# Kernel tuning notes

Hardware: AMD Instinct MI355X
Metric: run time of the kernel (lower is better)

## Reference

```python
import jax, jax.numpy as jnp
import numpy as np

TOP_K = 3


def setup_inputs() -> dict:
    key = jax.random.key(0)
    k1, k2, k3 = jax.random.split(key, 3)
    N, M, D = 100000, 6890, 128
    source_feats = jax.random.normal(k1, (N, D), dtype=jnp.float32)
    target_feats = jax.random.normal(k2, (M, D), dtype=jnp.float32)
    target_points = jax.random.normal(k3, (M, 3), dtype=jnp.float32)
    return {
        "source_feats": source_feats,
        "target_feats": target_feats,
        "target_points": target_points,
    }


def reference(source_feats, target_feats, target_points):
    # Pairwise squared distances via matmul + squared norms: [N, M]
    dp = jnp.matmul(source_feats, target_feats.T)
    source_sq = jnp.sum(source_feats * source_feats, axis=-1, keepdims=True)  # [N,1]
    target_sq = jnp.sum(target_feats * target_feats, axis=-1)                 # [M]
    dists = source_sq - 2.0 * dp + target_sq[None, :]
    # top-3 nearest neighbors (topk of negated distances, like torch.topk(-dists))
    scores, indices = jax.lax.top_k(-dists, TOP_K)      # [N,3], [N,3]
    weights = jax.nn.softmax(scores, axis=-1)           # [N,3]
    selected = target_points[indices]                   # [N,3,3] gather
    predicted_points = jnp.sum(selected * weights[..., None], axis=-2)  # [N,3]
    return predicted_points
```

## Files before the change

### kernel.cpp

```cpp
#include <hip/hip_runtime.h>
#include <math.h>

#define D 128
#define CT 2
#define SRCS_PER_WAVE (CT * 16)
#define WAVES 4
#define BIAS 16.0f
#define REFK 10
#define TILEB 8192
#define BUFB  8448

typedef __attribute__((ext_vector_type(8))) short short8;
typedef __attribute__((ext_vector_type(4))) float f32x4;

static __device__ __forceinline__ unsigned short f2bf(float x) {
    unsigned u = __float_as_uint(x);
    unsigned r = u + 0x7FFFu + ((u >> 16) & 1u);
    return (unsigned short)(r >> 16);
}

static __device__ __forceinline__ unsigned med3u(unsigned a, unsigned b, unsigned c) {
    unsigned d;
    asm("v_med3_u32 %0, %1, %2, %3" : "=v"(d) : "v"(a), "v"(b), "v"(c));
    return d;
}

static __device__ __forceinline__ void ins5(unsigned st[5], unsigned k) {
    st[4] = med3u(st[4], st[3], k);
    st[3] = med3u(st[3], st[2], k);
    st[2] = med3u(st[2], st[1], k);
    st[1] = med3u(st[1], st[0], k);
    st[0] = st[0] < k ? st[0] : k;
}

static __device__ __forceinline__ void ins10(unsigned st[REFK], unsigned k) {
    #pragma unroll
    for (int s = REFK - 1; s >= 1; --s) st[s] = med3u(st[s], st[s - 1], k);
    st[0] = st[0] < k ? st[0] : k;
}

static __device__ __forceinline__ void gload_lds16(const void* g, void* l) {
    __builtin_amdgcn_global_load_lds(
        (const __attribute__((address_space(1))) unsigned*)g,
        (__attribute__((address_space(3))) unsigned*)l, 16, 0, 0);
}
static __device__ __forceinline__ void gload_lds4(const void* g, void* l) {
    __builtin_amdgcn_global_load_lds(
        (const __attribute__((address_space(1))) unsigned*)g,
        (__attribute__((address_space(3))) unsigned*)l, 4, 0, 0);
}

__global__ void prep_kernel(const float* __restrict__ tgt, unsigned short* __restrict__ tbf,
                            float* __restrict__ tsqb, float* __restrict__ tsqe,
                            int M, int Mpad) {
    int row  = blockIdx.x;
    int lane = threadIdx.x;
    if (row >= Mpad) return;
    float2 v = make_float2(0.f, 0.f);
    if (row < M) v = *(const float2*)(tgt + (size_t)row * D + lane * 2);
    unsigned pack = (unsigned)f2bf(-2.f * v.x) | ((unsigned)f2bf(-2.f * v.y) << 16);
    size_t byte = (size_t)row * 256 + (size_t)(((lane >> 2) ^ (row & 15)) * 16 + (lane & 3) * 4);
    *(unsigned*)((char*)tbf + byte) = pack;
    float ss = v.x * v.x + v.y * v.y;
    #pragma unroll
    for (int off = 1; off < 64; off <<= 1) ss += __shfl_xor(ss, off);
    if (lane == 0) {
        tsqe[row] = ss;
        tsqb[row] = (row < M) ? (ss + BIAS) : __builtin_inff();
    }
}

__global__ __launch_bounds__(256, 4)
void knn_scan(const float* __restrict__ src, const unsigned short* __restrict__ tbf,
              const float* __restrict__ tsqb, unsigned* __restrict__ keys,
              int N, int M, int h0, int msteps) {
    const int tid  = (int)threadIdx.x;
    const int wid  = tid >> 6;
    const int lane = tid & 63;
    const int c16  = lane & 15;
    const int g    = lane >> 4;
    const int half = blockIdx.y;
    const int colbase = blockIdx.x * (WAVES * SRCS_PER_WAVE) + wid * SRCS_PER_WAVE;

    __shared__ __align__(16) char smem[3 * BUFB];

    short8 bfrag[CT][4];
    #pragma unroll
    for (int ct = 0; ct < CT; ++ct) {
        int srow = colbase + ct * 16 + c16;
        if (srow >= N) srow = N - 1;
        const float* sp = src + (size_t)srow * D + g * 8;
        #pragma unroll
        for (int kk = 0; kk < 4; ++kk) {
            float4 v0 = *(const float4*)(sp + kk * 32);
            float4 v1 = *(const float4*)(sp + kk * 32 + 4);
            short8 b;
            b[0] = (short)f2bf(v0.x); b[1] = (short)f2bf(v0.y);
            b[2] = (short)f2bf(v0.z); b[3] = (short)f2bf(v0.w);
            b[4] = (short)f2bf(v1.x); b[5] = (short)f2bf(v1.y);
            b[6] = (short)f2bf(v1.z); b[7] = (short)f2bf(v1.w);
            bfrag[ct][kk] = b;
        }
    }

    unsigned st[CT][5];
    #pragma unroll
    for (int ct = 0; ct < CT; ++ct)
        #pragma unroll
        for (int s = 0; s < 5; ++s) st[ct][s] = 0xFFFFFFFFu;

    int oe[4];
    #pragma unroll
    for (int kk = 0; kk < 4; ++kk) oe[kk] = c16 * 16 + ((g + 4 * kk) ^ c16);

    const int t0 = half ? h0 : 0;
    const int tc = half ? (msteps - h0) : h0;
    const int tlast = t0 + tc - 1;

    #define STAGE(tile, b)                                                          \
        do {                                                                        \
            const char* gb_ = (const char*)tbf + (size_t)(tile) * TILEB;            \
            char* lb_ = smem + (size_t)(b) * BUFB;                                  \
            gload_lds16(gb_ + wid * 2048 + lane * 16, lb_ + wid * 2048);            \
            gload_lds16(gb_ + wid * 2048 + 1024 + lane * 16, lb_ + wid * 2048 + 1024);\
            gload_lds4((const char*)tsqb + (size_t)(tile) * 128 + lane * 4,         \
                       lb_ + TILEB);                                                \
        } while (0)

    #define COMPUTE(b)                                                              \
        do {                                                                        \
            const short8* A_ = (const short8*)(smem + (size_t)(b) * BUFB);          \
            const float*  Q_ = (const float*)(smem + (size_t)(b) * BUFB + TILEB);   \
            _Pragma("unroll")                                                       \
            for (int sub_ = 0; sub_ < 2; ++sub_) {                                  \
                short8 a_[4];                                                       \
                _Pragma("unroll")                                                   \
                for (int kk = 0; kk < 4; ++kk) a_[kk] = A_[sub_ * 256 + oe[kk]];    \
                float4 q_ = *(const float4*)(Q_ + sub_ * 16 + g * 4);               \
                _Pragma("unroll")                                                   \
                for (int ct = 0; ct < CT; ++ct) {                                   \
                    f32x4 acc = { q_.x, q_.y, q_.z, q_.w };                         \
                    _Pragma("unroll")                                               \
                    for (int kk = 0; kk < 4; ++kk)                                  \
                        acc = __builtin_amdgcn_mfma_f32_16x16x32_bf16(              \
                                  a_[kk], bfrag[ct][kk], acc, 0, 0, 0);             \
                    _Pragma("unroll")                                               \
                    for (int e = 0; e < 4; ++e) {                                   \
                        unsigned key = (__float_as_uint(acc[e]) & 0xFFFFE000u)      \
                                       | (jb + (unsigned)e);                        \
                        ins5(st[ct], key);                                          \
                    }                                                               \
                }                                                                   \
                jb += 16;                                                           \
            }                                                                       \
        } while (0)

    unsigned jb = (unsigned)(t0 * 32 + g * 4);

    STAGE(t0, 0);
    STAGE(t0 + 1, 1);
    asm volatile("s_waitcnt vmcnt(3)\n\ts_barrier" ::: "memory");

    for (int i = 0; i < tc; i += 3) {
        int t_ = t0 + i;
        int s2 = t_ + 2 < tlast ? t_ + 2 : tlast;
        int s3 = t_ + 3 < tlast ? t_ + 3 : tlast;
        int s4 = t_ + 4 < tlast ? t_ + 4 : tlast;
        STAGE(s2, 2);
        COMPUTE(0);
        asm volatile("s_waitcnt vmcnt(3)\n\ts_barrier" ::: "memory");
        STAGE(s3, 0);
        COMPUTE(1);
        asm volatile("s_waitcnt vmcnt(3)\n\ts_barrier" ::: "memory");
        STAGE(s4, 1);
        COMPUTE(2);
        asm volatile("s_waitcnt vmcnt(3)\n\ts_barrier" ::: "memory");
    }
    asm volatile("s_waitcnt vmcnt(0)" ::: "memory");
    #undef STAGE
    #undef COMPUTE

    #pragma unroll
    for (int ct = 0; ct < CT; ++ct) {
        int srow = colbase + ct * 16 + c16;
        if (srow < N) {
            #pragma unroll
            for (int s = 0; s < 5; ++s)
                keys[(size_t)srow * 40 + half * 20 + g * 5 + s] = st[ct][s];
        }
    }
}

__global__ __launch_bounds__(256, 4)
void knn_merge(const float* __restrict__ src, const float* __restrict__ tgt,
               const float* __restrict__ tsqe, const unsigned* __restrict__ keys,
               const float* __restrict__ tpts, float* __restrict__ out,
               int N, int M) {
    int i = blockIdx.x * 256 + (int)threadIdx.x;
    if (i >= N) return;

    unsigned best[REFK];
    #pragma unroll
    for (int s = 0; s < REFK; ++s) best[s] = 0xFFFFFFFFu;

    const uint4* kp = (const uint4*)(keys + (size_t)i * 40);
    #pragma unroll
    for (int q = 0; q < 10; ++q) {
        uint4 kv = kp[q];
        ins10(best, kv.x); ins10(best, kv.y); ins10(best, kv.z); ins10(best, kv.w);
    }

    int js[REFK]; float dt[REFK];
    #pragma unroll
    for (int s = 0; s < REFK; ++s) {
        int j = (int)(best[s] & 0x1FFFu);
        js[s] = (j < M) ? j : (M - 1);
        dt[s] = 0.f;
    }

    const float4* sp = (const float4*)(src + (size_t)i * D);
    for (int kc = 0; kc < D / 4; ++kc) {
        float4 sv = sp[kc];
        #pragma unroll
        for (int s = 0; s < REFK; ++s) {
            float4 tv = *(const float4*)(tgt + (size_t)js[s] * D + kc * 4);
            dt[s] = fmaf(sv.x, tv.x, fmaf(sv.y, tv.y, fmaf(sv.z, tv.z, fmaf(sv.w, tv.w, dt[s]))));
        }
    }

    float d0 = __builtin_inff(), d1 = d0, d2 = d0;
    int i0 = 0, i1 = 0, i2 = 0;
    #pragma unroll
    for (int s = 0; s < REFK; ++s) {
        float dd = fmaf(-2.f, dt[s], tsqe[js[s]]);
        int jj = js[s];
        if (dd < d2) {
            if (dd < d1) {
                d2 = d1; i2 = i1;
                if (dd < d0) { d1 = d0; i1 = i0; d0 = dd; i0 = jj; }
                else         { d1 = dd; i1 = jj; }
            } else { d2 = dd; i2 = jj; }
        }
    }

    float e1 = __expf(d0 - d1);
    float e2 = __expf(d0 - d2);
    float inv = 1.f / (1.f + e1 + e2);
    float w0 = inv, w1 = e1 * inv, w2 = e2 * inv;
    const float* p0 = tpts + 3 * (size_t)i0;
    const float* p1 = tpts + 3 * (size_t)i1;
    const float* p2 = tpts + 3 * (size_t)i2;
    out[3 * (size_t)i + 0] = w0 * p0[0] + w1 * p1[0] + w2 * p2[0];
    out[3 * (size_t)i + 1] = w0 * p0[1] + w1 * p1[1] + w2 * p2[1];
    out[3 * (size_t)i + 2] = w0 * p0[2] + w1 * p1[2] + w2 * p2[2];
}

extern "C" void kernel_launch(void* const* d_in, const int* in_sizes, int n_in,
                              void* d_out, int out_size, void* d_ws, size_t ws_size,
                              hipStream_t stream) {
    const float* src  = (const float*)d_in[0];
    const float* tgt  = (const float*)d_in[1];
    const float* tpts = (const float*)d_in[2];
    float* out = (float*)d_out;

    int N = in_sizes[0] / D;
    int M = in_sizes[1] / D;
    int Mpad = (M + 191) & ~191;
    int msteps = Mpad >> 5;
    int h0 = msteps >> 1;

    char* w = (char*)d_ws;
    unsigned short* tbf = (unsigned short*)w;                 w += (size_t)Mpad * 256;
    float* tsqb = (float*)w;                                  w += (size_t)Mpad * 4;
    float* tsqe = (float*)w;                                  w += (size_t)Mpad * 4;
    unsigned* keys = (unsigned*)w;

    prep_kernel<<<Mpad, 64, 0, stream>>>(tgt, tbf, tsqb, tsqe, M, Mpad);

    int per_block = WAVES * SRCS_PER_WAVE;
    dim3 sgrid((N + per_block - 1) / per_block, 2);
    knn_scan<<<sgrid, 256, 0, stream>>>(src, tbf, tsqb, keys, N, M, h0, msteps);

    knn_merge<<<(N + 255) / 256, 256, 0, stream>>>(src, tgt, tsqe, keys, tpts, out, N, M);
}
```

Before: 417.1 us.

## Switch scan to 32x32x16 MFMA with bias folded into an extra MFMA

Replaces the 16x16x32 bf16 MFMA tiles (two column tiles per wave) with a single 32x32x16 MFMA per wave covering 32 sources. The per-target bias (norm plus offset) is now injected through an extra rank-2 MFMA that uses a hi/lo bf16 split of the bias against a constant B fragment, instead of initialising the accumulator from LDS. The LDS A-fragment addressing, the key index encoding and the merge decode are reworked to match the 32x32 output layout. This aims to raise MFMA efficiency and cut per-tile instruction overhead, at the cost of one extra MFMA per tile and bias precision limited by the bf16 hi/lo split. Top-k insertion now uses two 5-deep lists per lane over 16 accumulator values.

```diff
diff --git a/kernel.cpp b/kernel.cpp
--- a/kernel.cpp
+++ b/kernel.cpp
@@ -2,16 +2,16 @@
 #include <math.h>
 
 #define D 128
-#define CT 2
-#define SRCS_PER_WAVE (CT * 16)
 #define WAVES 4
 #define BIAS 16.0f
-#define REFK 10
 #define TILEB 8192
 #define BUFB  8448
+#define REFK 10
 
 typedef __attribute__((ext_vector_type(8))) short short8;
-typedef __attribute__((ext_vector_type(4))) float f32x4;
+typedef __attribute__((ext_vector_type(16))) float f32x16;
+
+union U8 { short8 s; unsigned u[4]; };
 
 static __device__ __forceinline__ unsigned short f2bf(float x) {
     unsigned u = __float_as_uint(x);
@@ -51,7 +51,7 @@
 }
 
 __global__ void prep_kernel(const float* __restrict__ tgt, unsigned short* __restrict__ tbf,
-                            float* __restrict__ tsqb, float* __restrict__ tsqe,
+                            unsigned* __restrict__ tshl, float* __restrict__ tsqe,
                             int M, int Mpad) {
     int row  = blockIdx.x;
     int lane = threadIdx.x;
@@ -66,52 +66,63 @@
     for (int off = 1; off < 64; off <<= 1) ss += __shfl_xor(ss, off);
     if (lane == 0) {
         tsqe[row] = ss;
-        tsqb[row] = (row < M) ? (ss + BIAS) : __builtin_inff();
+        float pv = (row < M) ? (ss + BIAS) : 1e30f;
+        unsigned hv = f2bf(pv);
+        float hf = __uint_as_float(hv << 16);
+        unsigned lv = f2bf(pv - hf);
+        int t = row >> 5, r = row & 31;
+        tshl[t * 64 + r]      = hv | (lv << 16);
+        tshl[t * 64 + 32 + r] = 0;
     }
 }
 
 __global__ __launch_bounds__(256, 4)
 void knn_scan(const float* __restrict__ src, const unsigned short* __restrict__ tbf,
-              const float* __restrict__ tsqb, unsigned* __restrict__ keys,
+              const unsigned* __restrict__ tshl, unsigned* __restrict__ keys,
               int N, int M, int h0, int msteps) {
     const int tid  = (int)threadIdx.x;
     const int wid  = tid >> 6;
     const int lane = tid & 63;
-    const int c16  = lane & 15;
-    const int g    = lane >> 4;
+    const int col  = lane & 31;
+    const int hi   = lane >> 5;
     const int half = blockIdx.y;
-    const int colbase = blockIdx.x * (WAVES * SRCS_PER_WAVE) + wid * SRCS_PER_WAVE;
+    const int colbase = blockIdx.x * (WAVES * 32) + wid * 32;
+    const int srow = colbase + col;
+    const int srcl = srow < N ? srow : (N - 1);
 
     __shared__ __align__(16) char smem[3 * BUFB];
 
-    short8 bfrag[CT][4];
-    #pragma unroll
-    for (int ct = 0; ct < CT; ++ct) {
-        int srow = colbase + ct * 16 + c16;
-        if (srow >= N) srow = N - 1;
-        const float* sp = src + (size_t)srow * D + g * 8;
+    short8 bfrag[8];
+    {
+        const float* sp = src + (size_t)srcl * D + hi * 8;
         #pragma unroll
-        for (int kk = 0; kk < 4; ++kk) {
-            float4 v0 = *(const float4*)(sp + kk * 32);
-            float4 v1 = *(const float4*)(sp + kk * 32 + 4);
+        for (int m = 0; m < 8; ++m) {
+            float4 v0 = *(const float4*)(sp + m * 16);
+            float4 v1 = *(const float4*)(sp + m * 16 + 4);
             short8 b;
             b[0] = (short)f2bf(v0.x); b[1] = (short)f2bf(v0.y);
             b[2] = (short)f2bf(v0.z); b[3] = (short)f2bf(v0.w);
             b[4] = (short)f2bf(v1.x); b[5] = (short)f2bf(v1.y);
             b[6] = (short)f2bf(v1.z); b[7] = (short)f2bf(v1.w);
-            bfrag[ct][kk] = b;
+            bfrag[m] = b;
         }
     }
 
-    unsigned st[CT][5];
-    #pragma unroll
-    for (int ct = 0; ct < CT; ++ct)
-        #pragma unroll
-        for (int s = 0; s < 5; ++s) st[ct][s] = 0xFFFFFFFFu;
-
-    int oe[4];
-    #pragma unroll
-    for (int kk = 0; kk < 4; ++kk) oe[kk] = c16 * 16 + ((g + 4 * kk) ^ c16);
+    U8 b2u; b2u.u[0] = hi ? 0u : 0x3F803F80u; b2u.u[1] = 0; b2u.u[2] = 0; b2u.u[3] = 0;
+
+    f32x16 zz;
+    #pragma unroll
+    for (int e = 0; e < 16; ++e) zz[e] = 0.f;
+
+    int aoff[8];
+    #pragma unroll
+    for (int m = 0; m < 8; ++m) aoff[m] = col * 256 + (((2 * m + hi) ^ (col & 15)) * 16);
+    const int toff = TILEB + col * 4 + hi * 128;
+
+    unsigned stA[5], stB[5];
+    #pragma unroll
+    for (int s = 0; s < 5; ++s) { stA[s] = 0xFFFFFFFFu; stB[s] = 0xFFFFFFFFu; }
+    const unsigned hib = (unsigned)(hi << 4);
 
     const int t0 = half ? h0 : 0;
     const int tc = half ? (msteps - h0) : h0;
@@ -123,39 +134,33 @@
             char* lb_ = smem + (size_t)(b) * BUFB;                                  \
             gload_lds16(gb_ + wid * 2048 + lane * 16, lb_ + wid * 2048);            \
             gload_lds16(gb_ + wid * 2048 + 1024 + lane * 16, lb_ + wid * 2048 + 1024);\
-            gload_lds4((const char*)tsqb + (size_t)(tile) * 128 + lane * 4,         \
+            gload_lds4((const char*)tshl + (size_t)(tile) * 256 + lane * 4,         \
                        lb_ + TILEB);                                                \
         } while (0)
 
-    #define COMPUTE(b)                                                              \
+    #define COMPUTE(b, tile)                                                        \
         do {                                                                        \
-            const short8* A_ = (const short8*)(smem + (size_t)(b) * BUFB);          \
-            const float*  Q_ = (const float*)(smem + (size_t)(b) * BUFB + TILEB);   \
+            const char* base_ = smem + (size_t)(b) * BUFB;                          \
+            unsigned pair_ = *(const unsigned*)(base_ + toff);                      \
+            U8 a2u_; a2u_.u[0] = pair_; a2u_.u[1] = 0; a2u_.u[2] = 0; a2u_.u[3] = 0;\
+            f32x16 acc = __builtin_amdgcn_mfma_f32_32x32x16_bf16(a2u_.s, b2u.s, zz, 0, 0, 0);\
             _Pragma("unroll")                                                       \
-            for (int sub_ = 0; sub_ < 2; ++sub_) {                                  \
-                short8 a_[4];                                                       \
-                _Pragma("unroll")                                                   \
-                for (int kk = 0; kk < 4; ++kk) a_[kk] = A_[sub_ * 256 + oe[kk]];    \
-                float4 q_ = *(const float4*)(Q_ + sub_ * 16 + g * 4);               \
-                _Pragma("unroll")                                                   \
-                for (int ct = 0; ct < CT; ++ct) {                                   \
-                    f32x4 acc = { q_.x, q_.y, q_.z, q_.w };                         \
-                    _Pragma("unroll")                                               \
-                    for (int kk = 0; kk < 4; ++kk)                                  \
-                        acc = __builtin_amdgcn_mfma_f32_16x16x32_bf16(              \
-                                  a_[kk], bfrag[ct][kk], acc, 0, 0, 0);             \
-                    _Pragma("unroll")                                               \
-                    for (int e = 0; e < 4; ++e) {                                   \
-                        unsigned key = (__float_as_uint(acc[e]) & 0xFFFFE000u)      \
-                                       | (jb + (unsigned)e);                        \
-                        ins5(st[ct], key);                                          \
-                    }                                                               \
-                }                                                                   \
-                jb += 16;                                                           \
+            for (int m = 0; m < 8; ++m) {                                           \
+                short8 am_ = *(const short8*)(base_ + aoff[m]);                     \
+                acc = __builtin_amdgcn_mfma_f32_32x32x16_bf16(am_, bfrag[m], acc, 0, 0, 0);\
+            }                                                                       \
+            unsigned vb_ = ((unsigned)(tile) << 5) | hib;                           \
+            _Pragma("unroll")                                                       \
+            for (int r = 0; r < 8; ++r) {                                           \
+                unsigned key_ = (__float_as_uint(acc[r]) & 0xFFFFE000u) | vb_ | (unsigned)r;\
+                ins5(stA, key_);                                                    \
+            }                                                                       \
+            _Pragma("unroll")                                                       \
+            for (int r = 8; r < 16; ++r) {                                          \
+                unsigned key_ = (__float_as_uint(acc[r]) & 0xFFFFE000u) | vb_ | (unsigned)r;\
+                ins5(stB, key_);                                                    \
             }                                                                       \
         } while (0)
-
-    unsigned jb = (unsigned)(t0 * 32 + g * 4);
 
     STAGE(t0, 0);
     STAGE(t0 + 1, 1);
@@ -167,27 +172,23 @@
         int s3 = t_ + 3 < tlast ? t_ + 3 : tlast;
         int s4 = t_ + 4 < tlast ? t_ + 4 : tlast;
         STAGE(s2, 2);
-        COMPUTE(0);
+        COMPUTE(0, t_);
         asm volatile("s_waitcnt vmcnt(3)\n\ts_barrier" ::: "memory");
         STAGE(s3, 0);
-        COMPUTE(1);
+        COMPUTE(1, t_ + 1);
         asm volatile("s_waitcnt vmcnt(3)\n\ts_barrier" ::: "memory");
         STAGE(s4, 1);
-        COMPUTE(2);
+        COMPUTE(2, t_ + 2);
         asm volatile("s_waitcnt vmcnt(3)\n\ts_barrier" ::: "memory");
     }
     asm volatile("s_waitcnt vmcnt(0)" ::: "memory");
     #undef STAGE
     #undef COMPUTE
 
-    #pragma unroll
-    for (int ct = 0; ct < CT; ++ct) {
-        int srow = colbase + ct * 16 + c16;
-        if (srow < N) {
-            #pragma unroll
-            for (int s = 0; s < 5; ++s)
-                keys[(size_t)srow * 40 + half * 20 + g * 5 + s] = st[ct][s];
-        }
+    if (srow < N) {
+        unsigned* kp = keys + (size_t)srow * 40 + half * 20 + hi * 10;
+        #pragma unroll
+        for (int s = 0; s < 5; ++s) { kp[s] = stA[s]; kp[5 + s] = stB[s]; }
     }
 }
 
@@ -213,8 +214,12 @@
     int js[REFK]; float dt[REFK];
     #pragma unroll
     for (int s = 0; s < REFK; ++s) {
-        int j = (int)(best[s] & 0x1FFFu);
-        js[s] = (j < M) ? j : (M - 1);
+        unsigned idx = best[s] & 0x1FFFu;
+        int tile = (int)(idx >> 5);
+        int hh   = (int)((idx >> 4) & 1u);
+        int reg  = (int)(idx & 15u);
+        int row  = tile * 32 + (reg & 3) + 8 * (reg >> 2) + 4 * hh;
+        js[s] = (row < M) ? row : (M - 1);
         dt[s] = 0.f;
     }
 
@@ -271,15 +276,14 @@
 
     char* w = (char*)d_ws;
     unsigned short* tbf = (unsigned short*)w;                 w += (size_t)Mpad * 256;
-    float* tsqb = (float*)w;                                  w += (size_t)Mpad * 4;
+    unsigned* tshl = (unsigned*)w;                            w += (size_t)msteps * 256;
     float* tsqe = (float*)w;                                  w += (size_t)Mpad * 4;
     unsigned* keys = (unsigned*)w;
 
-    prep_kernel<<<Mpad, 64, 0, stream>>>(tgt, tbf, tsqb, tsqe, M, Mpad);
-
-    int per_block = WAVES * SRCS_PER_WAVE;
-    dim3 sgrid((N + per_block - 1) / per_block, 2);
-    knn_scan<<<sgrid, 256, 0, stream>>>(src, tbf, tsqb, keys, N, M, h0, msteps);
+    prep_kernel<<<Mpad, 64, 0, stream>>>(tgt, tbf, tshl, tsqe, M, Mpad);
+
+    dim3 sgrid((N + 127) / 128, 2);
+    knn_scan<<<sgrid, 256, 0, stream>>>(src, tbf, tshl, keys, N, M, h0, msteps);
 
     knn_merge<<<(N + 255) / 256, 256, 0, stream>>>(src, tgt, tsqe, keys, tpts, out, N, M);
 }
```

New measurement: 402.1 us. -3.6%, faster.
